# Kernel tuning notes

Measured on AMD Instinct MI355X. Metric: run time of the kernel, lower is better.

## Reference

```python
import jax, jax.numpy as jnp
import numpy as np

N = 50000      # nodes
E = 800000     # edges
IN = 128       # in_channels
H = 256        # hidden_channels
EMB = 128      # embedding_size
R = 4          # num_relations
HEADS = 2


def setup_inputs() -> dict:
    key = jax.random.key(0)
    ks = jax.random.split(key, 20)
    w = lambda k, shape: jax.random.normal(k, shape, dtype=jnp.float32) * 0.05
    return dict(
        x=jax.random.normal(ks[0], (N, IN), dtype=jnp.float32),
        edge_index=jax.random.randint(ks[1], (2, E), 0, N, dtype=jnp.int32),
        edge_type=jax.random.randint(ks[2], (E,), 0, R, dtype=jnp.int32),
        sage1_Wl=w(ks[3], (IN, H)), sage1_Wr=w(ks[4], (IN, H)), sage1_b=jnp.zeros((H,), jnp.float32),
        sage2_Wl=w(ks[5], (H, H)), sage2_Wr=w(ks[6], (H, H)), sage2_b=jnp.zeros((H,), jnp.float32),
        gat_W=w(ks[7], (H, HEADS * H)), gat_att_src=w(ks[8], (HEADS, H)), gat_att_dst=w(ks[9], (HEADS, H)),
        gat_b=jnp.zeros((H,), jnp.float32),
        rgcn_Wrel=w(ks[10], (R, H, EMB)), rgcn_Wroot=w(ks[11], (H, EMB)), rgcn_b=jnp.zeros((EMB,), jnp.float32),
        fusion_W=w(ks[12], (H + H + EMB, EMB)), fusion_b=jnp.zeros((EMB,), jnp.float32),
    )


def _segmean(msg, seg, num_segments):
    s = jax.ops.segment_sum(msg, seg, num_segments=num_segments)
    c = jax.ops.segment_sum(jnp.ones((seg.shape[0], 1), msg.dtype), seg, num_segments=num_segments)
    return s / jnp.maximum(c, 1.0)


def _sage(x, src, dst, Wl, Wr, b, n):
    # SAGEConv: lin_l(mean_j x_j) + lin_r(x_i)
    agg = _segmean(x[src], dst, n)
    return agg @ Wl + x @ Wr + b


def _gat(x, src, dst, W, a_src, a_dst, b, n):
    # GATConv heads=2, concat=False (head average), add_self_loops=True
    loop = jnp.arange(n, dtype=src.dtype)
    src = jnp.concatenate([src, loop])
    dst = jnp.concatenate([dst, loop])
    h = (x @ W).reshape(n, HEADS, -1)                 # [N, heads, H]
    al_src = (h * a_src).sum(-1)                      # [N, heads]
    al_dst = (h * a_dst).sum(-1)                      # [N, heads]
    e = jax.nn.leaky_relu(al_src[src] + al_dst[dst], 0.2)   # [E', heads]
    m = jax.ops.segment_max(e, dst, num_segments=n)          # stable softmax per dst node
    ex = jnp.exp(e - m[dst])
    den = jax.ops.segment_sum(ex, dst, num_segments=n)
    alpha = ex / jnp.maximum(den[dst], 1e-16)
    out = jax.ops.segment_sum(alpha[:, :, None] * h[src], dst, num_segments=n)  # [N, heads, H]
    return out.mean(axis=1) + b


def _rgcn(x, src, dst, etype, Wrel, Wroot, b, n, r):
    # RGCNConv: sum_r mean_{j in N_r(i)} W_r x_j + W_root x_i + b
    xt = jnp.einsum('nh,rhe->rne', x, Wrel)           # [R, N, EMB]
    m = xt[etype, src]                                # [E, EMB]
    seg = dst * r + etype                             # per (node, relation) segment
    agg = _segmean(m, seg, n * r).reshape(n, r, -1).sum(axis=1)
    return agg + x @ Wroot + b


def reference(x, edge_index, edge_type,
              sage1_Wl, sage1_Wr, sage1_b,
              sage2_Wl, sage2_Wr, sage2_b,
              gat_W, gat_att_src, gat_att_dst, gat_b,
              rgcn_Wrel, rgcn_Wroot, rgcn_b,
              fusion_W, fusion_b):
    src, dst = edge_index[0], edge_index[1]
    n = x.shape[0]
    x1 = jax.nn.relu(_sage(x, src, dst, sage1_Wl, sage1_Wr, sage1_b, n))
    # dropout(p=0.2) is identity in eval mode
    x_sage = jax.nn.relu(_sage(x1, src, dst, sage2_Wl, sage2_Wr, sage2_b, n))
    x_gat = jax.nn.relu(_gat(x_sage, src, dst, gat_W, gat_att_src, gat_att_dst, gat_b, n))
    x_rgcn = _rgcn(x_gat, src, dst, edge_type, rgcn_Wrel, rgcn_Wroot, rgcn_b, n, R)
    x_all = jnp.concatenate([x_sage, x_gat, x_rgcn], axis=1)
    out = x_all @ fusion_W + fusion_b
    norm = jnp.maximum(jnp.linalg.norm(out, axis=1, keepdims=True), 1e-12)
    return out / norm
```

## Files before the change

### kernel.cpp

```cpp
#include <hip/hip_runtime.h>
#include <math.h>

constexpr int NN   = 50000;
constexpr int NE   = 800000;
constexpr int NREL = 4;
constexpr int NB   = (NN + 255) / 256;

typedef __attribute__((ext_vector_type(8))) short bfrag;
typedef __attribute__((ext_vector_type(4))) float floatx4;

__device__ inline unsigned short bf16_rne(float x) {
  unsigned u = __float_as_uint(x);
  unsigned r = (u + 0x7FFFu + ((u >> 16) & 1u)) >> 16;
  return (unsigned short)r;
}
__device__ inline float bf2f(unsigned short h) {
  return __uint_as_float((unsigned)h << 16);
}
__device__ inline void split2(float x, unsigned short& h, unsigned short& l) {
  h = bf16_rne(x);
  l = bf16_rne(x - bf2f(h));
}

__global__ void k_counts(const int* __restrict__ src, const int* __restrict__ dst,
                         const int* __restrict__ et, int* deg, int* cntrel) {
  int e = blockIdx.x * blockDim.x + threadIdx.x;
  if (e < NE) {
    int d = dst[e];
    atomicAdd(&deg[d], 1);
    atomicAdd(&cntrel[d * NREL + et[e]], 1);
  }
}

__global__ void k_scan1(const int* __restrict__ deg, int* bsum) {
  __shared__ int sm[256];
  int i = blockIdx.x * 256 + threadIdx.x;
  sm[threadIdx.x] = (i < NN) ? deg[i] : 0;
  __syncthreads();
  for (int s = 128; s; s >>= 1) {
    if (threadIdx.x < s) sm[threadIdx.x] += sm[threadIdx.x + s];
    __syncthreads();
  }
  if (threadIdx.x == 0) bsum[blockIdx.x] = sm[0];
}
__global__ void k_scan2(const int* __restrict__ bsum, int* boff, int* rowptr) {
  if (threadIdx.x == 0 && blockIdx.x == 0) {
    int acc = 0;
    for (int b = 0; b < NB; ++b) { boff[b] = acc; acc += bsum[b]; }
    rowptr[NN] = NE;
  }
}
__global__ void k_scan3(const int* __restrict__ deg, const int* __restrict__ boff,
                        int* rowptr) {
  __shared__ int sm[256];
  int i = blockIdx.x * 256 + threadIdx.x;
  int v = (i < NN) ? deg[i] : 0;
  sm[threadIdx.x] = v;
  __syncthreads();
  for (int s = 1; s < 256; s <<= 1) {
    int t = (threadIdx.x >= s) ? sm[threadIdx.x - s] : 0;
    __syncthreads();
    sm[threadIdx.x] += t;
    __syncthreads();
  }
  if (i < NN) rowptr[i] = boff[blockIdx.x] + sm[threadIdx.x] - v;
}

__global__ void k_fill(const int* __restrict__ src, const int* __restrict__ dst,
                       const int* __restrict__ et, const int* __restrict__ rowptr,
                       int* cursor, int* srcs, int* ets) {
  int e = blockIdx.x * blockDim.x + threadIdx.x;
  if (e >= NE) return;
  int d = dst[e];
  int pos = rowptr[d] + atomicAdd(&cursor[d], 1);
  srcs[pos] = src[e];
  ets[pos]  = et[e];
}

#define PK_N 14
__device__ __constant__ const int PK_BASE[PK_N]  = {0,1,2,3,4,4,5,5,5,5,6,7,7,7};
__device__ __constant__ const int PK_EOFF[PK_N]  = {0,0,0,0,0,256,0,32768,65536,98304,0,0,32768,65536};
__device__ __constant__ const int PK_K[PK_N]     = {128,128,256,256,256,256,256,256,256,256,256,256,256,128};
__device__ __constant__ const int PK_LDB[PK_N]   = {256,256,256,256,512,512,128,128,128,128,128,128,128,128};
__device__ __constant__ const int PK_START[PK_N] = {0,4096,8192,16384,24576,32768,40960,45056,49152,53248,57344,61440,65536,69632};
constexpr int PK_TOTAL = 71680;
constexpr int BF_S1WL = 0,     BF_S1WR = 4096,  BF_S2WL = 8192,  BF_S2WR = 16384;
constexpr int BF_GATW0 = 24576, BF_GATW1 = 32768, BF_WREL = 40960, BF_WROOT = 57344;
constexpr int BF_FW0 = 61440,  BF_FW1 = 65536,  BF_FW2 = 69632;

__global__ void k_pack(const float* b0, const float* b1, const float* b2, const float* b3,
                       const float* b4, const float* b5, const float* b6, const float* b7,
                       unsigned short* __restrict__ Bh) {
  int f = blockIdx.x * 256 + threadIdx.x;
  if (f >= PK_TOTAL) return;
  int m = 0;
#pragma unroll
  for (int i = 1; i < PK_N; ++i) if (f >= PK_START[i]) m = i;
  const float* bases[8] = {b0,b1,b2,b3,b4,b5,b6,b7};
  int lf = f - PK_START[m];
  int K = PK_K[m], ldb = PK_LDB[m];
  int Kq16 = K << 1;
  int ntile = lf / Kq16;
  int rem = lf - ntile * Kq16;
  int kq = rem >> 4, c = rem & 15;
  const float* sp = bases[PK_BASE[m]] + PK_EOFF[m] + (size_t)(kq * 8) * ldb + ntile * 16 + c;
#pragma unroll
  for (int j = 0; j < 8; ++j)
    Bh[(size_t)f * 8 + j] = bf16_rne(sp[(size_t)j * ldb]);
}

__global__ void k_split(const float* __restrict__ x, unsigned short* __restrict__ xh,
                        unsigned short* __restrict__ xl, long total4) {
  long i = (long)blockIdx.x * blockDim.x + threadIdx.x;
  if (i >= total4) return;
  float4 v = ((const float4*)x)[i];
  ushort4 h, l;
  split2(v.x, h.x, l.x); split2(v.y, h.y, l.y);
  split2(v.z, h.z, l.z); split2(v.w, h.w, l.w);
  ((ushort4*)xh)[i] = h;
  ((ushort4*)xl)[i] = l;
}

__global__ void k_mean128p(const unsigned short* __restrict__ ih, const int* __restrict__ rowptr,
                           const int* __restrict__ srcs,
                           unsigned short* __restrict__ oh, unsigned short* __restrict__ ol) {
  int node = blockIdx.x * 4 + (threadIdx.x >> 6);
  int lane = threadIdx.x & 63;
  if (node >= NN) return;
  int p0 = rowptr[node], p1 = rowptr[node + 1];
  float2 acc = make_float2(0.f, 0.f);
  int p = p0;
  for (; p + 4 <= p1; p += 4) {
    int s0 = srcs[p], s1 = srcs[p+1], s2 = srcs[p+2], s3 = srcs[p+3];
    ushort2 v0 = ((const ushort2*)(ih + ((size_t)s0 << 7)))[lane];
    ushort2 v1 = ((const ushort2*)(ih + ((size_t)s1 << 7)))[lane];
    ushort2 v2 = ((const ushort2*)(ih + ((size_t)s2 << 7)))[lane];
    ushort2 v3 = ((const ushort2*)(ih + ((size_t)s3 << 7)))[lane];
    acc.x += (bf2f(v0.x) + bf2f(v1.x)) + (bf2f(v2.x) + bf2f(v3.x));
    acc.y += (bf2f(v0.y) + bf2f(v1.y)) + (bf2f(v2.y) + bf2f(v3.y));
  }
  for (; p < p1; ++p) {
    int s = srcs[p];
    ushort2 hv = ((const ushort2*)(ih + ((size_t)s << 7)))[lane];
    acc.x += bf2f(hv.x); acc.y += bf2f(hv.y);
  }
  float inv = (p1 > p0) ? 1.0f / (float)(p1 - p0) : 0.0f;
  ushort2 h, l;
  split2(acc.x * inv, h.x, l.x); split2(acc.y * inv, h.y, l.y);
  size_t o = ((size_t)node << 7) + lane * 2;
  *(ushort2*)(oh + o) = h;
  *(ushort2*)(ol + o) = l;
}

__global__ void k_mean256p(const unsigned short* __restrict__ ih, const int* __restrict__ rowptr,
                           const int* __restrict__ srcs,
                           unsigned short* __restrict__ oh, unsigned short* __restrict__ ol) {
  int node = blockIdx.x * 4 + (threadIdx.x >> 6);
  int lane = threadIdx.x & 63;
  if (node >= NN) return;
  int p0 = rowptr[node], p1 = rowptr[node + 1];
  float4 acc = make_float4(0.f, 0.f, 0.f, 0.f);
  int p = p0;
  for (; p + 8 <= p1; p += 8) {
    int ss[8]; ushort4 xr[8];
#pragma unroll
    for (int j = 0; j < 8; ++j) ss[j] = srcs[p + j];
#pragma unroll
    for (int j = 0; j < 8; ++j)
      xr[j] = *(const ushort4*)(ih + ((size_t)ss[j] << 8) + lane * 4);
#pragma unroll
    for (int j = 0; j < 8; ++j) {
      acc.x += bf2f(xr[j].x); acc.y += bf2f(xr[j].y);
      acc.z += bf2f(xr[j].z); acc.w += bf2f(xr[j].w);
    }
  }
  for (; p < p1; ++p) {
    int s = srcs[p];
    ushort4 hv = *(const ushort4*)(ih + ((size_t)s << 8) + lane * 4);
    acc.x += bf2f(hv.x); acc.y += bf2f(hv.y);
    acc.z += bf2f(hv.z); acc.w += bf2f(hv.w);
  }
  float inv = (p1 > p0) ? 1.0f / (float)(p1 - p0) : 0.0f;
  ushort4 h, l;
  split2(acc.x * inv, h.x, l.x); split2(acc.y * inv, h.y, l.y);
  split2(acc.z * inv, h.z, l.z); split2(acc.w * inv, h.w, l.w);
  size_t o = ((size_t)node << 8) + lane * 4;
  *(ushort4*)(oh + o) = h;
  *(ushort4*)(ol + o) = l;
}

__global__ __launch_bounds__(256)
void k_gemm_mfma(const unsigned short* __restrict__ Bph,
                 const unsigned short* A0h, const unsigned short* A0l, int lda0, int bf0, int K0,
                 const unsigned short* A1h, const unsigned short* A1l, int lda1, int bf1, int K1,
                 const unsigned short* A2h, const unsigned short* A2l, int lda2, int bf2, int K2,
                 const float* __restrict__ bias, float* Cf,
                 unsigned short* Ch, unsigned short* Cl,
                 int M, int Nc, float scale, int do_relu, int zsB, long zsC, int xtmode)
{
  __shared__ short Ash[8*64*8], Asl[8*64*8], Bsh[8*64*8];
  const int tid  = threadIdx.x;
  const int lane = tid & 63;
  const int wv   = tid >> 6;
  const int wm   = wv >> 1, wn = wv & 1;
  const int nwg = gridDim.x * gridDim.y;
  const int d   = blockIdx.x + gridDim.x * blockIdx.y;
  const int q   = nwg >> 3, r = nwg & 7;
  const int xcd = d & 7, di = d >> 3;
  const int wg  = (xcd < r ? xcd * (q + 1) : r * (q + 1) + (xcd - r) * q) + di;
  const int row0 = (wg / gridDim.x) * 128;
  const int col0 = (wg % gridDim.x) * 128;
  if (zsB) {
    bf0 += blockIdx.z * zsB;
    long zc = (long)blockIdx.z * zsC;
    if (Cf) Cf += zc;
    if (Ch) { Ch += zc; if (Cl) Cl += zc; }
  }

  floatx4 acc[4][4];
#pragma unroll
  for (int i = 0; i < 4; ++i)
#pragma unroll
    for (int j = 0; j < 4; ++j) acc[i][j] = 0;

  const int a_m = tid >> 1;
  const int a_h = tid & 1;
  const int b_nt = tid >> 5;
  const int b_rem = (tid << 1) & 63;

  const unsigned short* Aharr[3] = {A0h, A1h, A2h};
  const unsigned short* Alarr[3] = {A0l, A1l, A2l};
  const int ldaArr[3] = {lda0, lda1, lda2};
  const int bfArr[3]  = {bf0, bf1, bf2};
  const int Karr[3]   = {K0, K1, K2};

  for (int p = 0; p < 3; ++p) {
    const int K = Karr[p];
    if (K == 0) continue;
    const int lda = ldaArr[p];
    const bool arow_ok = (row0 + a_m) < M;
    const unsigned short* Arh = Aharr[p] + (size_t)(row0 + a_m) * lda + a_h * 16;
    const unsigned short* Arl = Alarr[p] + (size_t)(row0 + a_m) * lda + a_h * 16;
    const int Kq16 = K << 1;
    const int bbase = bfArr[p] + (col0 >> 4) * Kq16 + b_nt * Kq16 + b_rem;

    for (int kt = 0; kt < K; kt += 32) {
      bfrag ah0, ah1, al0, al1;
      if (arow_ok) {
        ah0 = *(const bfrag*)(Arh + kt);
        ah1 = *(const bfrag*)(Arh + kt + 8);
        al0 = *(const bfrag*)(Arl + kt);
        al1 = *(const bfrag*)(Arl + kt + 8);
      } else {
#pragma unroll
        for (int i = 0; i < 8; ++i) { ah0[i]=0; ah1[i]=0; al0[i]=0; al1[i]=0; }
      }
      const unsigned short* bp_h = Bph + (size_t)(bbase + (kt << 1)) * 8;
      bfrag bh0 = *(const bfrag*)bp_h;
      bfrag bh1 = *(const bfrag*)(bp_h + 8);

      __syncthreads();
      {
        int q2 = a_h * 2;
        int i0 = ((a_m >> 4) * 64 + ((a_m & 15) | (q2 << 4))) * 8;
        int i1 = ((a_m >> 4) * 64 + ((a_m & 15) | ((q2 + 1) << 4))) * 8;
        *(bfrag*)&Ash[i0] = ah0;  *(bfrag*)&Ash[i1] = ah1;
        *(bfrag*)&Asl[i0] = al0;  *(bfrag*)&Asl[i1] = al1;
      }
      {
        int f0 = tid * 2;
        *(bfrag*)&Bsh[(size_t)f0 * 8] = bh0;
        *(bfrag*)&Bsh[(size_t)(f0 + 1) * 8] = bh1;
      }
      __syncthreads();

      bfrag afh[4], afl[4], bfh[4];
#pragma unroll
      for (int mt = 0; mt < 4; ++mt) {
        int idx = ((wm * 4 + mt) * 64 + lane) * 8;
        afh[mt] = *(bfrag*)&Ash[idx];
        afl[mt] = *(bfrag*)&Asl[idx];
      }
#pragma unroll
      for (int nt = 0; nt < 4; ++nt) {
        int idx = ((wn * 4 + nt) * 64 + lane) * 8;
        bfh[nt] = *(bfrag*)&Bsh[idx];
      }
#pragma unroll
      for (int mt = 0; mt < 4; ++mt)
#pragma unroll
        for (int nt = 0; nt < 4; ++nt) {
          acc[mt][nt] = __builtin_amdgcn_mfma_f32_16x16x32_bf16(afh[mt], bfh[nt], acc[mt][nt], 0, 0, 0);
          acc[mt][nt] = __builtin_amdgcn_mfma_f32_16x16x32_bf16(afl[mt], bfh[nt], acc[mt][nt], 0, 0, 0);
        }
    }
  }

  const int cl = lane & 15;
  const int rq = lane >> 4;
#pragma unroll
  for (int mt = 0; mt < 4; ++mt)
#pragma unroll
    for (int r2 = 0; r2 < 4; ++r2) {
      int row = row0 + wm * 64 + mt * 16 + rq * 4 + r2;
      if (row < M) {
#pragma unroll
        for (int nt = 0; nt < 4; ++nt) {
          int colx = col0 + wn * 64 + nt * 16 + cl;
          float vraw = acc[mt][nt][r2] * scale;
          if (xtmode == 2) {
            if (colx < 512) {
              size_t o = (size_t)(colx >> 7) * ((size_t)NN * 128) + (size_t)row * 128 + (colx & 127);
              Ch[o] = bf16_rne(vraw);
            } else {
              size_t o = (size_t)row * 128 + (colx & 127);
              Cf[o] = vraw + (bias ? bias[colx & 127] : 0.0f);
            }
          } else {
            float v = vraw + (bias ? bias[colx] : 0.0f);
            if (do_relu) v = fmaxf(v, 0.0f);
            size_t o = (size_t)row * Nc + colx;
            if (Cf) Cf[o] = v;
            if (Ch) {
              if (Cl) {
                unsigned short h, l; split2(v, h, l);
                Ch[o] = h; Cl[o] = l;
              } else {
                Ch[o] = bf16_rne(v);
              }
            }
          }
        }
      }
    }
}

__global__ void k_wtilde(const float* __restrict__ gatW, const float* __restrict__ att_s,
                         const float* __restrict__ att_d, float* __restrict__ wt) {
  int k = threadIdx.x;
  const float* Wr = gatW + (size_t)k * 512;
  float s0 = 0, s1 = 0, d0 = 0, d1 = 0;
  for (int i = 0; i < 256; ++i) {
    float w0 = Wr[i], w1 = Wr[256 + i];
    s0 += w0 * att_s[i];       s1 += w1 * att_s[256 + i];
    d0 += w0 * att_d[i];       d1 += w1 * att_d[256 + i];
  }
  wt[k] = s0; wt[256 + k] = s1; wt[512 + k] = d0; wt[768 + k] = d1;
}

__global__ void k_al(const unsigned short* __restrict__ xsh_, const float* __restrict__ wt,
                     float* __restrict__ al_s, float* __restrict__ al_d) {
  int node = blockIdx.x * 4 + (threadIdx.x >> 6);
  int lane = threadIdx.x & 63;
  if (node >= NN) return;
  ushort4 hv = *(const ushort4*)(xsh_ + (size_t)node * 256 + lane * 4);
  float4 v = make_float4(bf2f(hv.x), bf2f(hv.y), bf2f(hv.z), bf2f(hv.w));
  const float4* w = (const float4*)wt;
  float4 a0 = w[lane], a1 = w[64 + lane], a2 = w[128 + lane], a3 = w[192 + lane];
  float s0 = v.x*a0.x + v.y*a0.y + v.z*a0.z + v.w*a0.w;
  float s1 = v.x*a1.x + v.y*a1.y + v.z*a1.z + v.w*a1.w;
  float s2 = v.x*a2.x + v.y*a2.y + v.z*a2.z + v.w*a2.w;
  float s3 = v.x*a3.x + v.y*a3.y + v.z*a3.z + v.w*a3.w;
  for (int off = 32; off; off >>= 1) {
    s0 += __shfl_down(s0, off); s1 += __shfl_down(s1, off);
    s2 += __shfl_down(s2, off); s3 += __shfl_down(s3, off);
  }
  if (lane == 0) {
    al_s[node*2] = s0; al_s[node*2 + 1] = s1;
    al_d[node*2] = s2; al_d[node*2 + 1] = s3;
  }
}

__device__ inline float lrelu(float v) { return v > 0.f ? v : 0.2f * v; }

__global__ void k_gat_csr(const unsigned short* __restrict__ xsh_,
                          const int* __restrict__ rowptr, const int* __restrict__ srcs,
                          const float* __restrict__ als, const float* __restrict__ ald,
                          float2* __restrict__ es,
                          unsigned short* __restrict__ aggh, unsigned short* __restrict__ aggl) {
  int node = blockIdx.x * 4 + (threadIdx.x >> 6);
  int lane = threadIdx.x & 63;
  if (node >= NN) return;
  int p0 = rowptr[node], p1 = rowptr[node + 1];
  float bd0 = ald[node*2], bd1 = ald[node*2 + 1];
  float vs0 = lrelu(als[node*2] + bd0);
  float vs1 = lrelu(als[node*2 + 1] + bd1);

  float t0 = 0.f, t1 = 0.f;
  for (int p = p0 + lane; p < p1; p += 64) {
    int s = srcs[p];
    float2 a = *(const float2*)(als + (size_t)s * 2);
    float e0 = __expf(lrelu(a.x + bd0));
    float e1 = __expf(lrelu(a.y + bd1));
    es[p] = make_float2(e0, e1);
    t0 += e0; t1 += e1;
  }
  for (int off = 32; off; off >>= 1) {
    t0 += __shfl_xor(t0, off);
    t1 += __shfl_xor(t1, off);
  }
  float w0 = __expf(vs0), w1 = __expf(vs1);
  float den0 = t0 + w0, den1 = t1 + w1;
  __threadfence_block();

  ushort4 hv = *(const ushort4*)(xsh_ + (size_t)node * 256 + lane * 4);
  float4 v = make_float4(bf2f(hv.x), bf2f(hv.y), bf2f(hv.z), bf2f(hv.w));
  float4 acc0 = make_float4(w0*v.x, w0*v.y, w0*v.z, w0*v.w);
  float4 acc1 = make_float4(w1*v.x, w1*v.y, w1*v.z, w1*v.w);
  int p = p0;
  for (; p + 8 <= p1; p += 8) {
    int ss[8]; float2 ee[8]; ushort4 xr[8];
#pragma unroll
    for (int j = 0; j < 8; ++j) ss[j] = srcs[p + j];
#pragma unroll
    for (int j = 0; j < 8; ++j) ee[j] = es[p + j];
#pragma unroll
    for (int j = 0; j < 8; ++j)
      xr[j] = *(const ushort4*)(xsh_ + (size_t)ss[j] * 256 + lane * 4);
#pragma unroll
    for (int j = 0; j < 8; ++j) {
      float4 xv = make_float4(bf2f(xr[j].x), bf2f(xr[j].y), bf2f(xr[j].z), bf2f(xr[j].w));
      acc0.x += ee[j].x*xv.x; acc0.y += ee[j].x*xv.y;
      acc0.z += ee[j].x*xv.z; acc0.w += ee[j].x*xv.w;
      acc1.x += ee[j].y*xv.x; acc1.y += ee[j].y*xv.y;
      acc1.z += ee[j].y*xv.z; acc1.w += ee[j].y*xv.w;
    }
  }
  for (; p < p1; ++p) {
    int s = srcs[p];
    float2 e = es[p];
    ushort4 xh4 = *(const ushort4*)(xsh_ + (size_t)s * 256 + lane * 4);
    float4 xv = make_float4(bf2f(xh4.x), bf2f(xh4.y), bf2f(xh4.z), bf2f(xh4.w));
    acc0.x += e.x*xv.x; acc0.y += e.x*xv.y; acc0.z += e.x*xv.z; acc0.w += e.x*xv.w;
    acc1.x += e.y*xv.x; acc1.y += e.y*xv.y; acc1.z += e.y*xv.z; acc1.w += e.y*xv.w;
  }
  float i0 = 1.0f / fmaxf(den0, 1e-16f);
  float i1 = 1.0f / fmaxf(den1, 1e-16f);
  ushort4 h, l;
  size_t o = (size_t)node * 512 + lane * 4;
  split2(acc0.x*i0, h.x, l.x); split2(acc0.y*i0, h.y, l.y);
  split2(acc0.z*i0, h.z, l.z); split2(acc0.w*i0, h.w, l.w);
  *(ushort4*)(aggh + o) = h; *(ushort4*)(aggl + o) = l;
  split2(acc1.x*i1, h.x, l.x); split2(acc1.y*i1, h.y, l.y);
  split2(acc1.z*i1, h.z, l.z); split2(acc1.w*i1, h.w, l.w);
  *(ushort4*)(aggh + o + 256) = h; *(ushort4*)(aggl + o + 256) = l;
}

__global__ void k_rgcn_csr(const unsigned short* __restrict__ xth,
                           const int* __restrict__ rowptr, const int* __restrict__ srcs,
                           const int* __restrict__ ets, const int* __restrict__ cntrel,
                           const float* __restrict__ P3f,
                           unsigned short* __restrict__ oh, unsigned short* __restrict__ ol) {
  int node = blockIdx.x * 4 + (threadIdx.x >> 6);
  int lane = threadIdx.x & 63;
  if (node >= NN) return;
  int p0 = rowptr[node], p1 = rowptr[node + 1];
  float inv0, inv1, inv2, inv3;
  {
    int c0 = cntrel[node*NREL], c1 = cntrel[node*NREL+1];
    int c2 = cntrel[node*NREL+2], c3 = cntrel[node*NREL+3];
    inv0 = c0 ? 1.0f/(float)c0 : 0.0f;  inv1 = c1 ? 1.0f/(float)c1 : 0.0f;
    inv2 = c2 ? 1.0f/(float)c2 : 0.0f;  inv3 = c3 ? 1.0f/(float)c3 : 0.0f;
  }
  float2 acc = ((const float2*)(P3f + ((size_t)node << 7)))[lane];
  int p = p0;
  for (; p + 8 <= p1; p += 8) {
    int ss[8], rr[8]; ushort2 xr[8];
#pragma unroll
    for (int j = 0; j < 8; ++j) { ss[j] = srcs[p + j]; rr[j] = ets[p + j]; }
#pragma unroll
    for (int j = 0; j < 8; ++j)
      xr[j] = *(const ushort2*)(xth + (((size_t)rr[j] * NN + ss[j]) << 7) + lane * 2);
#pragma unroll
    for (int j = 0; j < 8; ++j) {
      float w = (rr[j] == 0) ? inv0 : (rr[j] == 1) ? inv1 : (rr[j] == 2) ? inv2 : inv3;
      acc.x += bf2f(xr[j].x) * w;
      acc.y += bf2f(xr[j].y) * w;
    }
  }
  for (; p < p1; ++p) {
    int s = srcs[p], r = ets[p];
    ushort2 hv = *(const ushort2*)(xth + (((size_t)r * NN + s) << 7) + lane * 2);
    float w = (r == 0) ? inv0 : (r == 1) ? inv1 : (r == 2) ? inv2 : inv3;
    acc.x += bf2f(hv.x) * w;
    acc.y += bf2f(hv.y) * w;
  }
  ushort2 h, l;
  split2(acc.x, h.x, l.x); split2(acc.y, h.y, l.y);
  size_t o = ((size_t)node << 7) + lane * 2;
  *(ushort2*)(oh + o) = h;
  *(ushort2*)(ol + o) = l;
}

__global__ void k_norm(float* __restrict__ out) {
  int gw = (int)(((long)blockIdx.x * blockDim.x + threadIdx.x) >> 6);
  int lane = threadIdx.x & 63;
  if (gw >= NN) return;
  float2* row = (float2*)(out + (size_t)gw * 128);
  float2 v = row[lane];
  float ss = v.x*v.x + v.y*v.y;
  for (int off = 32; off; off >>= 1) ss += __shfl_down(ss, off);
  ss = __shfl(ss, 0);
  float inv = 1.0f / fmaxf(sqrtf(ss), 1e-12f);
  row[lane] = make_float2(v.x*inv, v.y*inv);
}

extern "C" void kernel_launch(void* const* d_in, const int* in_sizes, int n_in,
                              void* d_out, int out_size, void* d_ws, size_t ws_size,
                              hipStream_t stream)
{
  const float* x     = (const float*)d_in[0];
  const int*   ei    = (const int*)d_in[1];
  const int*   etype = (const int*)d_in[2];
  const float* s1Wl  = (const float*)d_in[3];
  const float* s1Wr  = (const float*)d_in[4];
  const float* s1b   = (const float*)d_in[5];
  const float* s2Wl  = (const float*)d_in[6];
  const float* s2Wr  = (const float*)d_in[7];
  const float* s2b   = (const float*)d_in[8];
  const float* gatW  = (const float*)d_in[9];
  const float* att_s = (const float*)d_in[10];
  const float* att_d = (const float*)d_in[11];
  const float* gatb  = (const float*)d_in[12];
  const float* Wrel  = (const float*)d_in[13];
  const float* Wroot = (const float*)d_in[14];
  const float* rgcnb = (const float*)d_in[15];
  const float* fW    = (const float*)d_in[16];
  const float* fb    = (const float*)d_in[17];
  float* out = (float*)d_out;

  const int* src = ei;
  const int* dst = ei + NE;

  char* ws = (char*)d_ws;
  size_t off = 0;
  auto alloc = [&](size_t bytes) -> void* {
    void* p = ws + off;
    off = (off + bytes + 255) & ~(size_t)255;
    return p;
  };
  int*      deg    = (int*)alloc((size_t)NN * 4);
  int*      cntrel = (int*)alloc((size_t)NN * NREL * 4);
  int*      rowptr = (int*)alloc((size_t)(NN + 1) * 4);
  int*      cursor = (int*)alloc((size_t)NN * 4);
  int*      bsum   = (int*)alloc((size_t)NB * 4);
  int*      boff   = (int*)alloc((size_t)NB * 4);
  int*      srcs   = (int*)alloc((size_t)NE * 4);
  int*      ets    = (int*)alloc((size_t)NE * 4);
  float*    al_s   = (float*)alloc((size_t)NN * 2 * 4);
  float*    al_d   = (float*)alloc((size_t)NN * 2 * 4);
  float*    wt     = (float*)alloc((size_t)4 * 256 * 4);
  unsigned short* PBh = (unsigned short*)alloc((size_t)PK_TOTAL * 8 * 2);
  char* SAb = (char*)alloc((size_t)NN * 1024);
  char* SBb = (char*)alloc((size_t)NN * 1024);
  char* SCb = (char*)alloc((size_t)NN * 1024);
  char* SDb = (char*)alloc((size_t)NN * 1024);
  (void)ws_size; (void)in_sizes; (void)n_in; (void)out_size;

  unsigned short* xh  = (unsigned short*)SAb;
  unsigned short* xl  = xh + (size_t)NN * 128;
  unsigned short* m1h = xl + (size_t)NN * 128;
  unsigned short* m1l = m1h + (size_t)NN * 128;
  unsigned short* aggh = (unsigned short*)SAb;
  float*          P3f  = (float*)SAb;
  unsigned short* p3h  = (unsigned short*)(SAb + (size_t)NN * 512);
  unsigned short* p3l  = p3h + (size_t)NN * 128;
  unsigned short* x1h = (unsigned short*)SBb;
  unsigned short* x1l = x1h + (size_t)NN * 256;
  unsigned short* aggl = (unsigned short*)SBb;
  unsigned short* xth = (unsigned short*)SBb;
  unsigned short* m2h = (unsigned short*)SCb;
  unsigned short* m2l = m2h + (size_t)NN * 256;
  float2*         es  = (float2*)SCb;
  unsigned short* xgh = (unsigned short*)SCb;
  unsigned short* xgl = xgh + (size_t)NN * 256;
  unsigned short* xsh = (unsigned short*)SDb;
  unsigned short* xsl = xsh + (size_t)NN * 256;

  const int NODEB = (NN + 3) / 4;
  const int GY = (NN + 127) / 128;

  k_pack<<<(PK_TOTAL + 255) / 256, 256, 0, stream>>>(s1Wl, s1Wr, s2Wl, s2Wr, gatW, Wrel, Wroot, fW, PBh);
  hipMemsetAsync(deg, 0, (size_t)NN * 4, stream);
  hipMemsetAsync(cntrel, 0, (size_t)NN * NREL * 4, stream);
  hipMemsetAsync(cursor, 0, (size_t)NN * 4, stream);
  k_counts<<<(NE + 255) / 256, 256, 0, stream>>>(src, dst, etype, deg, cntrel);
  k_scan1<<<NB, 256, 0, stream>>>(deg, bsum);
  k_scan2<<<1, 64, 0, stream>>>(bsum, boff, rowptr);
  k_scan3<<<NB, 256, 0, stream>>>(deg, boff, rowptr);
  k_fill<<<(NE + 255) / 256, 256, 0, stream>>>(src, dst, etype, rowptr, cursor, srcs, ets);
  k_split<<<((NN * 128 / 4) + 255) / 256, 256, 0, stream>>>(x, xh, xl, (long)NN * 128 / 4);

  k_mean128p<<<NODEB, 256, 0, stream>>>(xh, rowptr, srcs, m1h, m1l);
  k_gemm_mfma<<<dim3(2, GY, 1), 256, 0, stream>>>(PBh,
      m1h, m1l, 128, BF_S1WL, 128,  xh, xl, 128, BF_S1WR, 128,  nullptr, nullptr, 0, 0, 0,
      s1b, nullptr, x1h, x1l, NN, 256, 1.0f, 1, 0, 0, 0);

  k_mean256p<<<NODEB, 256, 0, stream>>>(x1h, rowptr, srcs, m2h, m2l);
  k_gemm_mfma<<<dim3(2, GY, 1), 256, 0, stream>>>(PBh,
      m2h, m2l, 256, BF_S2WL, 256,  x1h, x1l, 256, BF_S2WR, 256,  nullptr, nullptr, 0, 0, 0,
      s2b, nullptr, xsh, xsl, NN, 256, 1.0f, 1, 0, 0, 0);

  k_wtilde<<<1, 256, 0, stream>>>(gatW, att_s, att_d, wt);
  k_al<<<NODEB, 256, 0, stream>>>(xsh, wt, al_s, al_d);
  k_gat_csr<<<NODEB, 256, 0, stream>>>(xsh, rowptr, srcs, al_s, al_d, es, aggh, aggl);
  k_gemm_mfma<<<dim3(2, GY, 1), 256, 0, stream>>>(PBh,
      aggh, aggl, 512, BF_GATW0, 256,  aggh + 256, aggl + 256, 512, BF_GATW1, 256,
      nullptr, nullptr, 0, 0, 0,
      gatb, nullptr, xgh, xgl, NN, 256, 0.5f, 1, 0, 0, 0);

  k_gemm_mfma<<<dim3(5, GY, 1), 256, 0, stream>>>(PBh,
      xgh, xgl, 256, BF_WREL, 256,  nullptr, nullptr, 0, 0, 0,  nullptr, nullptr, 0, 0, 0,
      rgcnb, P3f, xth, nullptr, NN, 640, 1.0f, 0, 0, 0, 2);
  k_rgcn_csr<<<NODEB, 256, 0, stream>>>(xth, rowptr, srcs, ets, cntrel, P3f, p3h, p3l);

  k_gemm_mfma<<<dim3(1, GY, 1), 256, 0, stream>>>(PBh,
      xsh, xsl, 256, BF_FW0, 256,  xgh, xgl, 256, BF_FW1, 256,  p3h, p3l, 128, BF_FW2, 128,
      fb, out, nullptr, nullptr, NN, 128, 1.0f, 0, 0, 0, 0);
  k_norm<<<(NN + 3) / 4, 256, 0, stream>>>(out);
}
```

Baseline: 830.5 us.

## Move bf16 hi/lo split from activations to weights and drop activation low halves

Activations are now stored only as a single bf16 value, and the weights carry the hi/lo pair instead. The GEMM now computes A_hi*B_hi + A_hi*B_lo rather than A_hi*B_hi + A_lo*B_hi. This removes the low-half activation buffers and their reads and writes in every gather and GEMM kernel, roughly halving activation memory traffic. It also folds the per-node degree count into the per-relation counts to save one atomic per edge. The cost is lower accuracy, because activation rounding error is no longer compensated.

Measured after the change: 750.2 us. 9.7% less time.

```diff
diff --git a/kernel.cpp b/kernel.cpp
--- a/kernel.cpp
+++ b/kernel.cpp
@@ -17,25 +17,22 @@
 __device__ inline float bf2f(unsigned short h) {
   return __uint_as_float((unsigned)h << 16);
 }
-__device__ inline void split2(float x, unsigned short& h, unsigned short& l) {
-  h = bf16_rne(x);
-  l = bf16_rne(x - bf2f(h));
-}
-
-__global__ void k_counts(const int* __restrict__ src, const int* __restrict__ dst,
-                         const int* __restrict__ et, int* deg, int* cntrel) {
+
+__global__ void k_counts(const int* __restrict__ dst, const int* __restrict__ et,
+                         int* cntrel) {
   int e = blockIdx.x * blockDim.x + threadIdx.x;
   if (e < NE) {
     int d = dst[e];
-    atomicAdd(&deg[d], 1);
     atomicAdd(&cntrel[d * NREL + et[e]], 1);
   }
 }
 
-__global__ void k_scan1(const int* __restrict__ deg, int* bsum) {
+__global__ void k_scan1(const int* __restrict__ cntrel, int* bsum) {
   __shared__ int sm[256];
   int i = blockIdx.x * 256 + threadIdx.x;
-  sm[threadIdx.x] = (i < NN) ? deg[i] : 0;
+  int v = 0;
+  if (i < NN) { int4 c = ((const int4*)cntrel)[i]; v = c.x + c.y + c.z + c.w; }
+  sm[threadIdx.x] = v;
   __syncthreads();
   for (int s = 128; s; s >>= 1) {
     if (threadIdx.x < s) sm[threadIdx.x] += sm[threadIdx.x + s];
@@ -50,11 +47,12 @@
     rowptr[NN] = NE;
   }
 }
-__global__ void k_scan3(const int* __restrict__ deg, const int* __restrict__ boff,
+__global__ void k_scan3(const int* __restrict__ cntrel, const int* __restrict__ boff,
                         int* rowptr) {
   __shared__ int sm[256];
   int i = blockIdx.x * 256 + threadIdx.x;
-  int v = (i < NN) ? deg[i] : 0;
+  int v = 0;
+  if (i < NN) { int4 c = ((const int4*)cntrel)[i]; v = c.x + c.y + c.z + c.w; }
   sm[threadIdx.x] = v;
   __syncthreads();
   for (int s = 1; s < 256; s <<= 1) {
@@ -90,7 +88,7 @@
 
 __global__ void k_pack(const float* b0, const float* b1, const float* b2, const float* b3,
                        const float* b4, const float* b5, const float* b6, const float* b7,
-                       unsigned short* __restrict__ Bh) {
+                       unsigned short* __restrict__ Bh, unsigned short* __restrict__ Bl) {
   int f = blockIdx.x * 256 + threadIdx.x;
   if (f >= PK_TOTAL) return;
   int m = 0;
@@ -105,25 +103,28 @@
   int kq = rem >> 4, c = rem & 15;
   const float* sp = bases[PK_BASE[m]] + PK_EOFF[m] + (size_t)(kq * 8) * ldb + ntile * 16 + c;
 #pragma unroll
-  for (int j = 0; j < 8; ++j)
-    Bh[(size_t)f * 8 + j] = bf16_rne(sp[(size_t)j * ldb]);
+  for (int j = 0; j < 8; ++j) {
+    float w = sp[(size_t)j * ldb];
+    unsigned short hh = bf16_rne(w);
+    Bh[(size_t)f * 8 + j] = hh;
+    Bl[(size_t)f * 8 + j] = bf16_rne(w - bf2f(hh));
+  }
 }
 
 __global__ void k_split(const float* __restrict__ x, unsigned short* __restrict__ xh,
-                        unsigned short* __restrict__ xl, long total4) {
+                        long total4) {
   long i = (long)blockIdx.x * blockDim.x + threadIdx.x;
   if (i >= total4) return;
   float4 v = ((const float4*)x)[i];
-  ushort4 h, l;
-  split2(v.x, h.x, l.x); split2(v.y, h.y, l.y);
-  split2(v.z, h.z, l.z); split2(v.w, h.w, l.w);
+  ushort4 h;
+  h.x = bf16_rne(v.x); h.y = bf16_rne(v.y);
+  h.z = bf16_rne(v.z); h.w = bf16_rne(v.w);
   ((ushort4*)xh)[i] = h;
-  ((ushort4*)xl)[i] = l;
 }
 
 __global__ void k_mean128p(const unsigned short* __restrict__ ih, const int* __restrict__ rowptr,
                            const int* __restrict__ srcs,
-                           unsigned short* __restrict__ oh, unsigned short* __restrict__ ol) {
+                           unsigned short* __restrict__ oh) {
   int node = blockIdx.x * 4 + (threadIdx.x >> 6);
   int lane = threadIdx.x & 63;
   if (node >= NN) return;
@@ -145,16 +146,15 @@
     acc.x += bf2f(hv.x); acc.y += bf2f(hv.y);
   }
   float inv = (p1 > p0) ? 1.0f / (float)(p1 - p0) : 0.0f;
-  ushort2 h, l;
-  split2(acc.x * inv, h.x, l.x); split2(acc.y * inv, h.y, l.y);
+  ushort2 h;
+  h.x = bf16_rne(acc.x * inv); h.y = bf16_rne(acc.y * inv);
   size_t o = ((size_t)node << 7) + lane * 2;
   *(ushort2*)(oh + o) = h;
-  *(ushort2*)(ol + o) = l;
 }
 
 __global__ void k_mean256p(const unsigned short* __restrict__ ih, const int* __restrict__ rowptr,
                            const int* __restrict__ srcs,
-                           unsigned short* __restrict__ oh, unsigned short* __restrict__ ol) {
+                           unsigned short* __restrict__ oh) {
   int node = blockIdx.x * 4 + (threadIdx.x >> 6);
   int lane = threadIdx.x & 63;
   if (node >= NN) return;
@@ -181,24 +181,23 @@
     acc.z += bf2f(hv.z); acc.w += bf2f(hv.w);
   }
   float inv = (p1 > p0) ? 1.0f / (float)(p1 - p0) : 0.0f;
-  ushort4 h, l;
-  split2(acc.x * inv, h.x, l.x); split2(acc.y * inv, h.y, l.y);
-  split2(acc.z * inv, h.z, l.z); split2(acc.w * inv, h.w, l.w);
+  ushort4 h;
+  h.x = bf16_rne(acc.x * inv); h.y = bf16_rne(acc.y * inv);
+  h.z = bf16_rne(acc.z * inv); h.w = bf16_rne(acc.w * inv);
   size_t o = ((size_t)node << 8) + lane * 4;
   *(ushort4*)(oh + o) = h;
-  *(ushort4*)(ol + o) = l;
 }
 
 __global__ __launch_bounds__(256)
 void k_gemm_mfma(const unsigned short* __restrict__ Bph,
-                 const unsigned short* A0h, const unsigned short* A0l, int lda0, int bf0, int K0,
-                 const unsigned short* A1h, const unsigned short* A1l, int lda1, int bf1, int K1,
-                 const unsigned short* A2h, const unsigned short* A2l, int lda2, int bf2, int K2,
-                 const float* __restrict__ bias, float* Cf,
-                 unsigned short* Ch, unsigned short* Cl,
-                 int M, int Nc, float scale, int do_relu, int zsB, long zsC, int xtmode)
+                 const unsigned short* __restrict__ Bpl,
+                 const unsigned short* A0, int lda0, int bf0, int K0,
+                 const unsigned short* A1, int lda1, int bf1, int K1,
+                 const unsigned short* A2, int lda2, int bf2, int K2,
+                 const float* __restrict__ bias, float* Cf, unsigned short* Ch,
+                 int M, int Nc, float scale, int do_relu, int xtmode)
 {
-  __shared__ short Ash[8*64*8], Asl[8*64*8], Bsh[8*64*8];
+  __shared__ short Ash[8*64*8], Bsh[8*64*8], Bsl[8*64*8];
   const int tid  = threadIdx.x;
   const int lane = tid & 63;
   const int wv   = tid >> 6;
@@ -210,12 +209,6 @@
   const int wg  = (xcd < r ? xcd * (q + 1) : r * (q + 1) + (xcd - r) * q) + di;
   const int row0 = (wg / gridDim.x) * 128;
   const int col0 = (wg % gridDim.x) * 128;
-  if (zsB) {
-    bf0 += blockIdx.z * zsB;
-    long zc = (long)blockIdx.z * zsC;
-    if (Cf) Cf += zc;
-    if (Ch) { Ch += zc; if (Cl) Cl += zc; }
-  }
 
   floatx4 acc[4][4];
 #pragma unroll
@@ -228,8 +221,7 @@
   const int b_nt = tid >> 5;
   const int b_rem = (tid << 1) & 63;
 
-  const unsigned short* Aharr[3] = {A0h, A1h, A2h};
-  const unsigned short* Alarr[3] = {A0l, A1l, A2l};
+  const unsigned short* Aarr[3] = {A0, A1, A2};
   const int ldaArr[3] = {lda0, lda1, lda2};
   const int bfArr[3]  = {bf0, bf1, bf2};
   const int Karr[3]   = {K0, K1, K2};
@@ -239,25 +231,24 @@
     if (K == 0) continue;
     const int lda = ldaArr[p];
     const bool arow_ok = (row0 + a_m) < M;
-    const unsigned short* Arh = Aharr[p] + (size_t)(row0 + a_m) * lda + a_h * 16;
-    const unsigned short* Arl = Alarr[p] + (size_t)(row0 + a_m) * lda + a_h * 16;
+    const unsigned short* Ar = Aarr[p] + (size_t)(row0 + a_m) * lda + a_h * 16;
     const int Kq16 = K << 1;
     const int bbase = bfArr[p] + (col0 >> 4) * Kq16 + b_nt * Kq16 + b_rem;
 
     for (int kt = 0; kt < K; kt += 32) {
-      bfrag ah0, ah1, al0, al1;
+      bfrag ah0, ah1;
       if (arow_ok) {
-        ah0 = *(const bfrag*)(Arh + kt);
-        ah1 = *(const bfrag*)(Arh + kt + 8);
-        al0 = *(const bfrag*)(Arl + kt);
-        al1 = *(const bfrag*)(Arl + kt + 8);
+        ah0 = *(const bfrag*)(Ar + kt);
+        ah1 = *(const bfrag*)(Ar + kt + 8);
       } else {
 #pragma unroll
-        for (int i = 0; i < 8; ++i) { ah0[i]=0; ah1[i]=0; al0[i]=0; al1[i]=0; }
+        for (int i = 0; i < 8; ++i) { ah0[i]=0; ah1[i]=0; }
       }
-      const unsigned short* bp_h = Bph + (size_t)(bbase + (kt << 1)) * 8;
-      bfrag bh0 = *(const bfrag*)bp_h;
-      bfrag bh1 = *(const bfrag*)(bp_h + 8);
+      const size_t boff = (size_t)(bbase + (kt << 1)) * 8;
+      bfrag bh0 = *(const bfrag*)(Bph + boff);
+      bfrag bh1 = *(const bfrag*)(Bph + boff + 8);
+      bfrag bl0 = *(const bfrag*)(Bpl + boff);
+      bfrag bl1 = *(const bfrag*)(Bpl + boff + 8);
 
       __syncthreads();
       {
@@ -265,33 +256,34 @@
         int i0 = ((a_m >> 4) * 64 + ((a_m & 15) | (q2 << 4))) * 8;
         int i1 = ((a_m >> 4) * 64 + ((a_m & 15) | ((q2 + 1) << 4))) * 8;
         *(bfrag*)&Ash[i0] = ah0;  *(bfrag*)&Ash[i1] = ah1;
-        *(bfrag*)&Asl[i0] = al0;  *(bfrag*)&Asl[i1] = al1;
       }
       {
         int f0 = tid * 2;
         *(bfrag*)&Bsh[(size_t)f0 * 8] = bh0;
         *(bfrag*)&Bsh[(size_t)(f0 + 1) * 8] = bh1;
+        *(bfrag*)&Bsl[(size_t)f0 * 8] = bl0;
+        *(bfrag*)&Bsl[(size_t)(f0 + 1) * 8] = bl1;
       }
       __syncthreads();
 
-      bfrag afh[4], afl[4], bfh[4];
+      bfrag afh[4], bfh[4], bfl[4];
 #pragma unroll
       for (int mt = 0; mt < 4; ++mt) {
         int idx = ((wm * 4 + mt) * 64 + lane) * 8;
         afh[mt] = *(bfrag*)&Ash[idx];
-        afl[mt] = *(bfrag*)&Asl[idx];
       }
 #pragma unroll
       for (int nt = 0; nt < 4; ++nt) {
         int idx = ((wn * 4 + nt) * 64 + lane) * 8;
         bfh[nt] = *(bfrag*)&Bsh[idx];
+        bfl[nt] = *(bfrag*)&Bsl[idx];
       }
 #pragma unroll
       for (int mt = 0; mt < 4; ++mt)
 #pragma unroll
         for (int nt = 0; nt < 4; ++nt) {
           acc[mt][nt] = __builtin_amdgcn_mfma_f32_16x16x32_bf16(afh[mt], bfh[nt], acc[mt][nt], 0, 0, 0);
-          acc[mt][nt] = __builtin_amdgcn_mfma_f32_16x16x32_bf16(afl[mt], bfh[nt], acc[mt][nt], 0, 0, 0);
+          acc[mt][nt] = __builtin_amdgcn_mfma_f32_16x16x32_bf16(afh[mt], bfl[nt], acc[mt][nt], 0, 0, 0);
         }
     }
   }
@@ -321,14 +313,7 @@
             if (do_relu) v = fmaxf(v, 0.0f);
             size_t o = (size_t)row * Nc + colx;
             if (Cf) Cf[o] = v;
-            if (Ch) {
-              if (Cl) {
-                unsigned short h, l; split2(v, h, l);
-                Ch[o] = h; Cl[o] = l;
-              } else {
-                Ch[o] = bf16_rne(v);
-              }
-            }
+            if (Ch) Ch[o] = bf16_rne(v);
           }
         }
       }
@@ -377,7 +362,7 @@
                           const int* __restrict__ rowptr, const int* __restrict__ srcs,
                           const float* __restrict__ als, const float* __restrict__ ald,
                           float2* __restrict__ es,
-                          unsigned short* __restrict__ aggh, unsigned short* __restrict__ aggl) {
+                          unsigned short* __restrict__ aggh) {
   int node = blockIdx.x * 4 + (threadIdx.x >> 6);
   int lane = threadIdx.x & 63;
   if (node >= NN) return;
@@ -436,31 +421,30 @@
   }
   float i0 = 1.0f / fmaxf(den0, 1e-16f);
   float i1 = 1.0f / fmaxf(den1, 1e-16f);
-  ushort4 h, l;
+  ushort4 h;
   size_t o = (size_t)node * 512 + lane * 4;
-  split2(acc0.x*i0, h.x, l.x); split2(acc0.y*i0, h.y, l.y);
-  split2(acc0.z*i0, h.z, l.z); split2(acc0.w*i0, h.w, l.w);
-  *(ushort4*)(aggh + o) = h; *(ushort4*)(aggl + o) = l;
-  split2(acc1.x*i1, h.x, l.x); split2(acc1.y*i1, h.y, l.y);
-  split2(acc1.z*i1, h.z, l.z); split2(acc1.w*i1, h.w, l.w);
-  *(ushort4*)(aggh + o + 256) = h; *(ushort4*)(aggl + o + 256) = l;
+  h.x = bf16_rne(acc0.x*i0); h.y = bf16_rne(acc0.y*i0);
+  h.z = bf16_rne(acc0.z*i0); h.w = bf16_rne(acc0.w*i0);
+  *(ushort4*)(aggh + o) = h;
+  h.x = bf16_rne(acc1.x*i1); h.y = bf16_rne(acc1.y*i1);
+  h.z = bf16_rne(acc1.z*i1); h.w = bf16_rne(acc1.w*i1);
+  *(ushort4*)(aggh + o + 256) = h;
 }
 
 __global__ void k_rgcn_csr(const unsigned short* __restrict__ xth,
                            const int* __restrict__ rowptr, const int* __restrict__ srcs,
                            const int* __restrict__ ets, const int* __restrict__ cntrel,
                            const float* __restrict__ P3f,
-                           unsigned short* __restrict__ oh, unsigned short* __restrict__ ol) {
+                           unsigned short* __restrict__ oh) {
   int node = blockIdx.x * 4 + (threadIdx.x >> 6);
   int lane = threadIdx.x & 63;
   if (node >= NN) return;
   int p0 = rowptr[node], p1 = rowptr[node + 1];
   float inv0, inv1, inv2, inv3;
   {
-    int c0 = cntrel[node*NREL], c1 = cntrel[node*NREL+1];
-    int c2 = cntrel[node*NREL+2], c3 = cntrel[node*NREL+3];
-    inv0 = c0 ? 1.0f/(float)c0 : 0.0f;  inv1 = c1 ? 1.0f/(float)c1 : 0.0f;
-    inv2 = c2 ? 1.0f/(float)c2 : 0.0f;  inv3 = c3 ? 1.0f/(float)c3 : 0.0f;
+    int4 c = ((const int4*)cntrel)[node];
+    inv0 = c.x ? 1.0f/(float)c.x : 0.0f;  inv1 = c.y ? 1.0f/(float)c.y : 0.0f;
+    inv2 = c.z ? 1.0f/(float)c.z : 0.0f;  inv3 = c.w ? 1.0f/(float)c.w : 0.0f;
   }
   float2 acc = ((const float2*)(P3f + ((size_t)node << 7)))[lane];
   int p = p0;
@@ -485,11 +469,10 @@
     acc.x += bf2f(hv.x) * w;
     acc.y += bf2f(hv.y) * w;
   }
-  ushort2 h, l;
-  split2(acc.x, h.x, l.x); split2(acc.y, h.y, l.y);
+  ushort2 h;
+  h.x = bf16_rne(acc.x); h.y = bf16_rne(acc.y);
   size_t o = ((size_t)node << 7) + lane * 2;
   *(ushort2*)(oh + o) = h;
-  *(ushort2*)(ol + o) = l;
 }
 
 __global__ void k_norm(float* __restrict__ out) {
@@ -551,71 +534,62 @@
   float*    al_d   = (float*)alloc((size_t)NN * 2 * 4);
   float*    wt     = (float*)alloc((size_t)4 * 256 * 4);
   unsigned short* PBh = (unsigned short*)alloc((size_t)PK_TOTAL * 8 * 2);
+  unsigned short* PBl = (unsigned short*)alloc((size_t)PK_TOTAL * 8 * 2);
   char* SAb = (char*)alloc((size_t)NN * 1024);
   char* SBb = (char*)alloc((size_t)NN * 1024);
   char* SCb = (char*)alloc((size_t)NN * 1024);
   char* SDb = (char*)alloc((size_t)NN * 1024);
-  (void)ws_size; (void)in_sizes; (void)n_in; (void)out_size;
+  (void)deg; (void)ws_size; (void)in_sizes; (void)n_in; (void)out_size;
 
   unsigned short* xh  = (unsigned short*)SAb;
-  unsigned short* xl  = xh + (size_t)NN * 128;
-  unsigned short* m1h = xl + (size_t)NN * 128;
-  unsigned short* m1l = m1h + (size_t)NN * 128;
+  unsigned short* m1h = xh + (size_t)NN * 128;
   unsigned short* aggh = (unsigned short*)SAb;
   float*          P3f  = (float*)SAb;
   unsigned short* p3h  = (unsigned short*)(SAb + (size_t)NN * 512);
-  unsigned short* p3l  = p3h + (size_t)NN * 128;
   unsigned short* x1h = (unsigned short*)SBb;
-  unsigned short* x1l = x1h + (size_t)NN * 256;
-  unsigned short* aggl = (unsigned short*)SBb;
   unsigned short* xth = (unsigned short*)SBb;
   unsigned short* m2h = (unsigned short*)SCb;
-  unsigned short* m2l = m2h + (size_t)NN * 256;
   float2*         es  = (float2*)SCb;
   unsigned short* xgh = (unsigned short*)SCb;
-  unsigned short* xgl = xgh + (size_t)NN * 256;
   unsigned short* xsh = (unsigned short*)SDb;
-  unsigned short* xsl = xsh + (size_t)NN * 256;
 
   const int NODEB = (NN + 3) / 4;
   const int GY = (NN + 127) / 128;
 
-  k_pack<<<(PK_TOTAL + 255) / 256, 256, 0, stream>>>(s1Wl, s1Wr, s2Wl, s2Wr, gatW, Wrel, Wroot, fW, PBh);
-  hipMemsetAsync(deg, 0, (size_t)NN * 4, stream);
+  k_pack<<<(PK_TOTAL + 255) / 256, 256, 0, stream>>>(s1Wl, s1Wr, s2Wl, s2Wr, gatW, Wrel, Wroot, fW, PBh, PBl);
   hipMemsetAsync(cntrel, 0, (size_t)NN * NREL * 4, stream);
   hipMemsetAsync(cursor, 0, (size_t)NN * 4, stream);
-  k_counts<<<(NE + 255) / 256, 256, 0, stream>>>(src, dst, etype, deg, cntrel);
-  k_scan1<<<NB, 256, 0, stream>>>(deg, bsum);
+  k_counts<<<(NE + 255) / 256, 256, 0, stream>>>(dst, etype, cntrel);
+  k_scan1<<<NB, 256, 0, stream>>>(cntrel, bsum);
   k_scan2<<<1, 64, 0, stream>>>(bsum, boff, rowptr);
-  k_scan3<<<NB, 256, 0, stream>>>(deg, boff, rowptr);
+  k_scan3<<<NB, 256, 0, stream>>>(cntrel, boff, rowptr);
   k_fill<<<(NE + 255) / 256, 256, 0, stream>>>(src, dst, etype, rowptr, cursor, srcs, ets);
-  k_split<<<((NN * 128 / 4) + 255) / 256, 256, 0, stream>>>(x, xh, xl, (long)NN * 128 / 4);
-
-  k_mean128p<<<NODEB, 256, 0, stream>>>(xh, rowptr, srcs, m1h, m1l);
-  k_gemm_mfma<<<dim3(2, GY, 1), 256, 0, stream>>>(PBh,
-      m1h, m1l, 128, BF_S1WL, 128,  xh, xl, 128, BF_S1WR, 128,  nullptr, nullptr, 0, 0, 0,
-      s1b, nullptr, x1h, x1l, NN, 256, 1.0f, 1, 0, 0, 0);
-
-  k_mean256p<<<NODEB, 256, 0, stream>>>(x1h, rowptr, srcs, m2h, m2l);
-  k_gemm_mfma<<<dim3(2, GY, 1), 256, 0, stream>>>(PBh,
-      m2h, m2l, 256, BF_S2WL, 256,  x1h, x1l, 256, BF_S2WR, 256,  nullptr, nullptr, 0, 0, 0,
-      s2b, nullptr, xsh, xsl, NN, 256, 1.0f, 1, 0, 0, 0);
+  k_split<<<((NN * 128 / 4) + 255) / 256, 256, 0, stream>>>(x, xh, (long)NN * 128 / 4);
+
+  k_mean128p<<<NODEB, 256, 0, stream>>>(xh, rowptr, srcs, m1h);
+  k_gemm_mfma<<<dim3(2, GY, 1), 256, 0, stream>>>(PBh, PBl,
+      m1h, 128, BF_S1WL, 128,  xh, 128, BF_S1WR, 128,  nullptr, 0, 0, 0,
+      s1b, nullptr, x1h, NN, 256, 1.0f, 1, 0);
+
+  k_mean256p<<<NODEB, 256, 0, stream>>>(x1h, rowptr, srcs, m2h);
+  k_gemm_mfma<<<dim3(2, GY, 1), 256, 0, stream>>>(PBh, PBl,
+      m2h, 256, BF_S2WL, 256,  x1h, 256, BF_S2WR, 256,  nullptr, 0, 0, 0,
+      s2b, nullptr, xsh, NN, 256, 1.0f, 1, 0);
 
   k_wtilde<<<1, 256, 0, stream>>>(gatW, att_s, att_d, wt);
   k_al<<<NODEB, 256, 0, stream>>>(xsh, wt, al_s, al_d);
-  k_gat_csr<<<NODEB, 256, 0, stream>>>(xsh, rowptr, srcs, al_s, al_d, es, aggh, aggl);
-  k_gemm_mfma<<<dim3(2, GY, 1), 256, 0, stream>>>(PBh,
-      aggh, aggl, 512, BF_GATW0, 256,  aggh + 256, aggl + 256, 512, BF_GATW1, 256,
-      nullptr, nullptr, 0, 0, 0,
-      gatb, nullptr, xgh, xgl, NN, 256, 0.5f, 1, 0, 0, 0);
-
-  k_gemm_mfma<<<dim3(5, GY, 1), 256, 0, stream>>>(PBh,
-      xgh, xgl, 256, BF_WREL, 256,  nullptr, nullptr, 0, 0, 0,  nullptr, nullptr, 0, 0, 0,
-      rgcnb, P3f, xth, nullptr, NN, 640, 1.0f, 0, 0, 0, 2);
-  k_rgcn_csr<<<NODEB, 256, 0, stream>>>(xth, rowptr, srcs, ets, cntrel, P3f, p3h, p3l);
-
-  k_gemm_mfma<<<dim3(1, GY, 1), 256, 0, stream>>>(PBh,
-      xsh, xsl, 256, BF_FW0, 256,  xgh, xgl, 256, BF_FW1, 256,  p3h, p3l, 128, BF_FW2, 128,
-      fb, out, nullptr, nullptr, NN, 128, 1.0f, 0, 0, 0, 0);
+  k_gat_csr<<<NODEB, 256, 0, stream>>>(xsh, rowptr, srcs, al_s, al_d, es, aggh);
+  k_gemm_mfma<<<dim3(2, GY, 1), 256, 0, stream>>>(PBh, PBl,
+      aggh, 512, BF_GATW0, 256,  aggh + 256, 512, BF_GATW1, 256,  nullptr, 0, 0, 0,
+      gatb, nullptr, xgh, NN, 256, 0.5f, 1, 0);
+
+  k_gemm_mfma<<<dim3(5, GY, 1), 256, 0, stream>>>(PBh, PBl,
+      xgh, 256, BF_WREL, 256,  nullptr, 0, 0, 0,  nullptr, 0, 0, 0,
+      rgcnb, P3f, xth, NN, 640, 1.0f, 0, 2);
+  k_rgcn_csr<<<NODEB, 256, 0, stream>>>(xth, rowptr, srcs, ets, cntrel, P3f, p3h);
+
+  k_gemm_mfma<<<dim3(1, GY, 1), 256, 0, stream>>>(PBh, PBl,
+      xsh, 256, BF_FW0, 256,  xgh, 256, BF_FW1, 256,  p3h, 128, BF_FW2, 128,
+      fb, out, nullptr, NN, 128, 1.0f, 0, 0);
   k_norm<<<(NN + 3) / 4, 256, 0, stream>>>(out);
 }
```
